# Optimization experiments

Measured on AMD Instinct MI355X. Metric: run time of the kernel, lower is better.

## Reference

```python
import jax, jax.numpy as jnp
import numpy as np

DIM_Q, DIM_K, HEADS = 256, 32, 4
SCALE = (DIM_Q // HEADS) ** (-0.5)


def setup_inputs() -> dict:
    key = jax.random.key(0)
    ks = jax.random.split(key, 12)
    B, C, H, W, D = 2, DIM_Q, 16, 16, 16
    inp = {
        'F_VNet': jax.random.normal(ks[0], (B, C, H, W, D), dtype=jnp.float32),
        'F_Knowledge': jax.random.normal(ks[1], (B, DIM_K, H, W, D), dtype=jnp.float32),
        # torch nn.Linear: y = x @ W.T + b, W: [out, in]
        'Wq': jax.random.normal(ks[2], (DIM_Q, DIM_Q), dtype=jnp.float32) * (DIM_Q ** -0.5),
        'bq': jnp.zeros((DIM_Q,), dtype=jnp.float32),
        'Wk': jax.random.normal(ks[3], (DIM_Q, DIM_K), dtype=jnp.float32) * (DIM_K ** -0.5),
        'bk': jnp.zeros((DIM_Q,), dtype=jnp.float32),
        'Wv': jax.random.normal(ks[4], (DIM_Q, DIM_K), dtype=jnp.float32) * (DIM_K ** -0.5),
        'bv': jnp.zeros((DIM_Q,), dtype=jnp.float32),
        'Wo': jax.random.normal(ks[5], (DIM_Q, DIM_Q), dtype=jnp.float32) * (DIM_Q ** -0.5),
        'bo': jnp.zeros((DIM_Q,), dtype=jnp.float32),
    }
    return inp


def reference(F_VNet, F_Knowledge, Wq, bq, Wk, bk, Wv, bv, Wo, bo):
    B, C, H, W, D = F_VNet.shape
    Ck = F_Knowledge.shape[1]
    # flatten spatial dims to tokens: [B, N, C]
    xq = F_VNet.reshape(B, C, -1).transpose(0, 2, 1)          # [B, Nq, dim_q]
    xk = F_Knowledge.reshape(B, Ck, -1).transpose(0, 2, 1)    # [B, Nk, dim_k]
    Q = xq @ Wq.T + bq                                        # [B, Nq, dim_q]
    K = xk @ Wk.T + bk                                        # [B, Nk, dim_q]
    V = xk @ Wv.T + bv                                        # [B, Nk, dim_q]
    attn = jax.nn.softmax(jnp.einsum('bqc,bkc->bqk', Q, K) * SCALE, axis=-1)
    out = jnp.einsum('bqk,bkc->bqc', attn, V)                 # [B, Nq, dim_q]
    out = out @ Wo.T + bo
    out = out.transpose(0, 2, 1).reshape(B, C, H, W, D)
    return F_VNet + out
```

## Files before the change

kernel.cpp:

```cpp
#include <hip/hip_runtime.h>
#include <hip/hip_bf16.h>
#include <cstdint>
#include <cstddef>

#define N_TOK 4096
#define CQ    256
#define CK    32
#define QK_SCALE 0.18033688011112042f

typedef __attribute__((ext_vector_type(4))) float  f32x4;
typedef __attribute__((ext_vector_type(8))) __bf16 bf16x8;
typedef __attribute__((ext_vector_type(4))) short  s16x4;

__device__ __forceinline__ unsigned short f2bf(float f) {
  union { float f; unsigned u; } x; x.f = f;
  unsigned r = x.u + 0x7FFFu + ((x.u >> 16) & 1u);
  return (unsigned short)(r >> 16);
}

__device__ __forceinline__ f32x4 mfma16(bf16x8 a, bf16x8 b, f32x4 c) {
  return __builtin_amdgcn_mfma_f32_16x16x32_bf16(a, b, c, 0, 0, 0);
}

__device__ __forceinline__ float exp2fast(float x) {
#if __has_builtin(__builtin_amdgcn_exp2f)
  return __builtin_amdgcn_exp2f(x);
#else
  float r; asm("v_exp_f32 %0, %1" : "=v"(r) : "v"(x)); return r;
#endif
}

__device__ __forceinline__ void bar_lds() {
  asm volatile("s_waitcnt lgkmcnt(0)" ::: "memory");
  __builtin_amdgcn_s_barrier();
}

__device__ __forceinline__ int pos2key(int pos) {
  return ((pos >> 3) << 2) + (pos & 3) + (((pos >> 2) & 1) << 4);
}

__global__ __launch_bounds__(256) void prep_kernel(
    const float* __restrict__ Wq, const float* __restrict__ bq,
    const float* __restrict__ Wk, const float* __restrict__ Wv,
    const float* __restrict__ bv, const float* __restrict__ Wo,
    const float* __restrict__ bo, const float* __restrict__ Fk,
    unsigned short* __restrict__ Aqkt, float* __restrict__ bqk,
    unsigned short* __restrict__ W2bf, float* __restrict__ c2,
    unsigned short* __restrict__ Vpv, unsigned short* __restrict__ XkT)
{
  __shared__ float red[256];
  __shared__ unsigned short trs[128][33];
  const int blk = blockIdx.x, t = threadIdx.x;
  if (blk < 32) {
    const int j = blk;
    float acc = 0.f;
    #pragma unroll 16
    for (int i = 0; i < CQ; i++)
      acc = fmaf(Wq[(size_t)i * CQ + t], Wk[(size_t)i * CK + j], acc);
    Aqkt[(size_t)j * CQ + t] = f2bf(QK_SCALE * acc);
    red[t] = bq[t] * Wk[(size_t)t * CK + j];
    __syncthreads();
    for (int s = 128; s > 0; s >>= 1) {
      if (t < s) red[t] += red[t + s];
      __syncthreads();
    }
    if (t == 0) bqk[j] = QK_SCALE * red[0];
  } else if (blk < 64) {
    const int j = blk - 32;
    float acc = 0.f, acc2 = 0.f;
    #pragma unroll 16
    for (int i = 0; i < CQ; i++) {
      float wo = Wo[(size_t)t * CQ + i];
      acc  = fmaf(wo, Wv[(size_t)i * CK + j], acc);
      acc2 = fmaf(wo, bv[i], acc2);
    }
    W2bf[(size_t)t * CK + j] = f2bf(acc);
    if (j == 0) c2[t] = bo[t] + acc2;
  } else {
    const int blk2 = blk - 64;
    const int b = blk2 >> 5;
    const int t0 = (blk2 & 31) << 7;
    #pragma unroll
    for (int i = 0; i < 4; i++) {
      int flat = (i * 256 + t) << 2;
      int r = flat >> 7, c4 = flat & 127;
      float4 v = *(const float4*)(Fk + ((size_t)(b * CK + r)) * N_TOK + t0 + c4);
      ushort4 u = { f2bf(v.x), f2bf(v.y), f2bf(v.z), f2bf(v.w) };
      trs[c4][r] = u.x; trs[c4+1][r] = u.y; trs[c4+2][r] = u.z; trs[c4+3][r] = u.w;
    }
    __syncthreads();
    {
      const int token = t >> 1, half = t & 1;
      unsigned short tmp[16] __attribute__((aligned(16)));
      #pragma unroll
      for (int k = 0; k < 16; k++) tmp[k] = trs[token][half * 16 + k];
      unsigned short* dst = XkT + ((size_t)(b * N_TOK + t0 + token)) * CK + half * 16;
      ((uint4*)dst)[0] = ((const uint4*)tmp)[0];
      ((uint4*)dst)[1] = ((const uint4*)tmp)[1];
    }
    {
      const int ch32l = t >> 6, d = (t & 63) >> 1, ph = t & 1;
      unsigned short tmp[16] __attribute__((aligned(16)));
      #pragma unroll
      for (int i = 0; i < 16; i++) {
        int pos = ph * 16 + i;
        tmp[i] = trs[ch32l * 32 + pos2key(pos)][d];
      }
      unsigned short* dst = Vpv +
          (((size_t)(b * 128 + (t0 >> 5) + ch32l)) * 32 + d) * 32 + ph * 16;
      ((uint4*)dst)[0] = ((const uint4*)tmp)[0];
      ((uint4*)dst)[1] = ((const uint4*)tmp)[1];
    }
  }
}

__global__ __launch_bounds__(256, 1) void fused_kernel(
    const float* __restrict__ X, const unsigned short* __restrict__ Aqkt,
    const float* __restrict__ bqk, const unsigned short* __restrict__ XkT,
    const unsigned short* __restrict__ Vpv,
    const unsigned short* __restrict__ W2bf, const float* __restrict__ c2,
    float* __restrict__ Y)
{
  __shared__ union {
    unsigned short ks[512 * 40];
    unsigned short bs8[8][32][40];
  } u __attribute__((aligned(16)));
  __shared__ unsigned short qn[32][40] __attribute__((aligned(16)));
  __shared__ float mlx[2][2][16];
  __shared__ float ofx[2][16][32];

  const int b  = blockIdx.x >> 7;
  const int t0 = (blockIdx.x & 127) << 5;
  const int t = threadIdx.x, w = t >> 6;
  const int lane = t & 63, c = lane & 15, g = lane >> 4;
  const int tw = w & 1, kh = w >> 1;
  const int pk = kh << 8;

  #pragma unroll
  for (int i = 0; i < 8; i++) {
    int flat = i * 256 + t;
    int cc = flat >> 3, tk = (flat & 7) << 2;
    float4 v = *(const float4*)(X + ((size_t)(b * CQ + cc)) * N_TOK + t0 + tk);
    int kk = cc >> 5, chl = cc & 31;
    u.bs8[kk][tk    ][chl] = f2bf(v.x);
    u.bs8[kk][tk + 1][chl] = f2bf(v.y);
    u.bs8[kk][tk + 2][chl] = f2bf(v.z);
    u.bs8[kk][tk + 3][chl] = f2bf(v.w);
  }
  const unsigned short* xksrc = XkT + ((size_t)b * N_TOK) * CK;
  uint4 R[8];
  #pragma unroll
  for (int r = 0; r < 8; r++)
    R[r] = *(const uint4*)(xksrc + (size_t)(r * 256 + t) * 8);
  bar_lds();

  if (w < 2) {
    f32x4 qacc[2] = {};
    #pragma unroll
    for (int kk = 0; kk < 8; kk++) {
      bf16x8 a = *(const bf16x8*)&u.bs8[kk][w * 16 + c][g * 8];
      #pragma unroll
      for (int nt = 0; nt < 2; nt++) {
        bf16x8 bB = *(const bf16x8*)(Aqkt + (size_t)(nt * 16 + c) * CQ + kk * 32 + g * 8);
        qacc[nt] = mfma16(a, bB, qacc[nt]);
      }
    }
    #pragma unroll
    for (int nt = 0; nt < 2; nt++) {
      float bj = bqk[nt * 16 + c];
      #pragma unroll
      for (int r = 0; r < 4; r++)
        qn[w * 16 + g * 4 + r][nt * 16 + c] = f2bf(qacc[nt][r] + bj);
    }
  }
  bar_lds();

  const bf16x8 qf = *(const bf16x8*)&qn[tw * 16 + c][g * 8];
  const unsigned short* vp = Vpv + (size_t)b * 128 * 1024;

  float mO = -1e30f, lO = 0.f;
  f32x4 O0 = {}, O1 = {};

  for (int s = 0; s < 8; s++) {
    #pragma unroll
    for (int r = 0; r < 8; r++) {
      int flat = r * 256 + t;
      *(uint4*)(u.ks + (flat >> 2) * 40 + (flat & 3) * 8) = R[r];
    }
    if (s < 7) {
      const unsigned short* nsrc = xksrc + (size_t)(s + 1) * (512 * CK);
      #pragma unroll
      for (int r = 0; r < 8; r++)
        R[r] = *(const uint4*)(nsrc + (size_t)(r * 256 + t) * 8);
    }
    bar_lds();

    f32x4 sc[4][4];
    #pragma unroll
    for (int it = 0; it < 4; it++)
      #pragma unroll
      for (int nt = 0; nt < 4; nt++) {
        bf16x8 ak = *(const bf16x8*)&u.ks[(pk + it * 64 + nt * 16 + c) * 40 + g * 8];
        f32x4 z = {};
        sc[it][nt] = mfma16(ak, qf, z);
      }

    float mx = -1e30f;
    #pragma unroll
    for (int it = 0; it < 4; it++)
      #pragma unroll
      for (int nt = 0; nt < 4; nt++)
        mx = fmaxf(mx, fmaxf(fmaxf(sc[it][nt][0], sc[it][nt][1]),
                             fmaxf(sc[it][nt][2], sc[it][nt][3])));
    mx = fmaxf(mx, __shfl_xor(mx, 16));
    mx = fmaxf(mx, __shfl_xor(mx, 32));

    float l = 0.f;
    s16x4 pf[4][4];
    #pragma unroll
    for (int it = 0; it < 4; it++)
      #pragma unroll
      for (int nt = 0; nt < 4; nt++) {
        float p0 = exp2fast(sc[it][nt][0] - mx);
        float p1 = exp2fast(sc[it][nt][1] - mx);
        float p2 = exp2fast(sc[it][nt][2] - mx);
        float p3 = exp2fast(sc[it][nt][3] - mx);
        l += (p0 + p1) + (p2 + p3);
        union { __hip_bfloat162 h2[2]; s16x4 v; } pu;
        pu.h2[0] = __float22bfloat162_rn(make_float2(p0, p1));
        pu.h2[1] = __float22bfloat162_rn(make_float2(p2, p3));
        pf[it][nt] = pu.v;
      }
    l += __shfl_xor(l, 16);
    l += __shfl_xor(l, 32);

    f32x4 o0 = {}, o1 = {};
    #pragma unroll
    for (int it = 0; it < 4; it++)
      #pragma unroll
      for (int ntp = 0; ntp < 2; ntp++) {
        const int ch32 = (s << 4) + (kh << 3) + it * 2 + ntp;
        const unsigned short* base = vp + (size_t)ch32 * 1024;
        union { s16x4 h[2]; bf16x8 v; } bu;
        bu.h[0] = pf[it][ntp * 2];
        bu.h[1] = pf[it][ntp * 2 + 1];
        bf16x8 a0 = *(const bf16x8*)(base + c * 32 + g * 8);
        bf16x8 a1 = *(const bf16x8*)(base + (16 + c) * 32 + g * 8);
        o0 = mfma16(a0, bu.v, o0);
        o1 = mfma16(a1, bu.v, o1);
      }

    float mN = fmaxf(mO, mx);
    float fO = exp2fast(mO - mN), fP = exp2fast(mx - mN);
    lO = lO * fO + l * fP;
    #pragma unroll
    for (int r = 0; r < 4; r++) {
      O0[r] = O0[r] * fO + o0[r] * fP;
      O1[r] = O1[r] * fO + o1[r] * fP;
    }
    mO = mN;
    bar_lds();
  }

  if (kh == 1) {
    if (lane < 16) { mlx[tw][0][c] = mO; mlx[tw][1][c] = lO; }
    #pragma unroll
    for (int r = 0; r < 4; r++) {
      ofx[tw][c][g * 4 + r]      = O0[r];
      ofx[tw][c][16 + g * 4 + r] = O1[r];
    }
  }
  __syncthreads();
  if (kh == 0) {
    float m1 = mlx[tw][0][c], l1 = mlx[tw][1][c];
    float mN = fmaxf(mO, m1);
    float f0 = exp2fast(mO - mN), f1 = exp2fast(m1 - mN);
    float inv = 1.0f / (lO * f0 + l1 * f1);
    f0 *= inv; f1 *= inv;
    #pragma unroll
    for (int r = 0; r < 4; r++) {
      qn[tw * 16 + c][g * 4 + r]      = f2bf(O0[r] * f0 + ofx[tw][c][g * 4 + r] * f1);
      qn[tw * 16 + c][16 + g * 4 + r] = f2bf(O1[r] * f0 + ofx[tw][c][16 + g * 4 + r] * f1);
    }
  }
  __syncthreads();

  const int m0 = w * 64;
  bf16x8 wb[2];
  #pragma unroll
  for (int nt = 0; nt < 2; nt++)
    wb[nt] = *(const bf16x8*)&qn[nt * 16 + c][g * 8];
  f32x4 acc2[4][2] = {};
  #pragma unroll
  for (int mt = 0; mt < 4; mt++) {
    bf16x8 aW = *(const bf16x8*)(W2bf + (size_t)(m0 + mt * 16 + c) * CK + g * 8);
    acc2[mt][0] = mfma16(aW, wb[0], acc2[mt][0]);
    acc2[mt][1] = mfma16(aW, wb[1], acc2[mt][1]);
  }
  #pragma unroll
  for (int mt = 0; mt < 4; mt++)
    #pragma unroll
    for (int r = 0; r < 4; r++) {
      const int row = m0 + mt * 16 + g * 4 + r;
      const float cc2 = c2[row];
      #pragma unroll
      for (int nt = 0; nt < 2; nt++) {
        size_t idx = ((size_t)(b * CQ + row)) * N_TOK + t0 + nt * 16 + c;
        Y[idx] = acc2[mt][nt][r] + cc2 + X[idx];
      }
    }
}

extern "C" void kernel_launch(void* const* d_in, const int* in_sizes, int n_in,
                              void* d_out, int out_size, void* d_ws, size_t ws_size,
                              hipStream_t stream) {
  const float* F  = (const float*)d_in[0];
  const float* Fk = (const float*)d_in[1];
  const float* Wq = (const float*)d_in[2];
  const float* bq = (const float*)d_in[3];
  const float* Wk = (const float*)d_in[4];
  const float* Wv = (const float*)d_in[6];
  const float* bv = (const float*)d_in[7];
  const float* Wo = (const float*)d_in[8];
  const float* bo = (const float*)d_in[9];
  float* Y = (float*)d_out;
  char* ws = (char*)d_ws;
  unsigned short* XkT   = (unsigned short*)(ws);
  unsigned short* Vpv   = (unsigned short*)(ws + (512u << 10));
  unsigned short* Aqkt  = (unsigned short*)(ws + (2048u << 10));
  unsigned short* W2bf  = (unsigned short*)(ws + (2080u << 10));
  float*          bqk   = (float*)(ws + (2112u << 10));
  float*          c2    = (float*)(ws + (2116u << 10));

  prep_kernel <<<128, 256, 0, stream>>>(Wq, bq, Wk, Wv, bv, Wo, bo, Fk,
                                        Aqkt, bqk, W2bf, c2, Vpv, XkT);
  fused_kernel<<<256, 256, 0, stream>>>(F, Aqkt, bqk, XkT, Vpv, W2bf, c2, Y);
}
```

Baseline: 120.6 us.

## Split keys across four waves with 16-query blocks and drop LDS K staging

Each block now handles 16 query tokens instead of 32, doubling the grid to 512 blocks. The four waves each take a quarter of the keys and read K fragments straight from global memory instead of staging them in LDS with barriers. The four partial softmax states are merged through LDS at the end. This cuts LDS use and per-iteration synchronisation to raise occupancy and parallelism, at the cost of redundant Q projection in every wave and uncoalesced global loads of X and K.

```diff
diff --git a/kernel.cpp b/kernel.cpp
--- a/kernel.cpp
+++ b/kernel.cpp
@@ -28,11 +28,6 @@
 #else
   float r; asm("v_exp_f32 %0, %1" : "=v"(r) : "v"(x)); return r;
 #endif
-}
-
-__device__ __forceinline__ void bar_lds() {
-  asm volatile("s_waitcnt lgkmcnt(0)" ::: "memory");
-  __builtin_amdgcn_s_barrier();
 }
 
 __device__ __forceinline__ int pos2key(int pos) {
@@ -114,93 +109,60 @@
   }
 }
 
-__global__ __launch_bounds__(256, 1) void fused_kernel(
+__global__ __launch_bounds__(256, 2) void fused_kernel(
     const float* __restrict__ X, const unsigned short* __restrict__ Aqkt,
     const float* __restrict__ bqk, const unsigned short* __restrict__ XkT,
     const unsigned short* __restrict__ Vpv,
     const unsigned short* __restrict__ W2bf, const float* __restrict__ c2,
     float* __restrict__ Y)
 {
-  __shared__ union {
-    unsigned short ks[512 * 40];
-    unsigned short bs8[8][32][40];
-  } u __attribute__((aligned(16)));
-  __shared__ unsigned short qn[32][40] __attribute__((aligned(16)));
-  __shared__ float mlx[2][2][16];
-  __shared__ float ofx[2][16][32];
-
-  const int b  = blockIdx.x >> 7;
-  const int t0 = (blockIdx.x & 127) << 5;
+  __shared__ unsigned short qn[16][40] __attribute__((aligned(16)));
+  __shared__ float ml[4][2][16];
+  __shared__ float ow[4][16][34];
+
+  const int b  = blockIdx.x >> 8;
+  const int t0 = (blockIdx.x & 255) << 4;
   const int t = threadIdx.x, w = t >> 6;
   const int lane = t & 63, c = lane & 15, g = lane >> 4;
-  const int tw = w & 1, kh = w >> 1;
-  const int pk = kh << 8;
-
-  #pragma unroll
-  for (int i = 0; i < 8; i++) {
-    int flat = i * 256 + t;
-    int cc = flat >> 3, tk = (flat & 7) << 2;
-    float4 v = *(const float4*)(X + ((size_t)(b * CQ + cc)) * N_TOK + t0 + tk);
-    int kk = cc >> 5, chl = cc & 31;
-    u.bs8[kk][tk    ][chl] = f2bf(v.x);
-    u.bs8[kk][tk + 1][chl] = f2bf(v.y);
-    u.bs8[kk][tk + 2][chl] = f2bf(v.z);
-    u.bs8[kk][tk + 3][chl] = f2bf(v.w);
-  }
-  const unsigned short* xksrc = XkT + ((size_t)b * N_TOK) * CK;
-  uint4 R[8];
-  #pragma unroll
-  for (int r = 0; r < 8; r++)
-    R[r] = *(const uint4*)(xksrc + (size_t)(r * 256 + t) * 8);
-  bar_lds();
-
-  if (w < 2) {
-    f32x4 qacc[2] = {};
-    #pragma unroll
-    for (int kk = 0; kk < 8; kk++) {
-      bf16x8 a = *(const bf16x8*)&u.bs8[kk][w * 16 + c][g * 8];
-      #pragma unroll
-      for (int nt = 0; nt < 2; nt++) {
-        bf16x8 bB = *(const bf16x8*)(Aqkt + (size_t)(nt * 16 + c) * CQ + kk * 32 + g * 8);
-        qacc[nt] = mfma16(a, bB, qacc[nt]);
-      }
-    }
+
+  f32x4 qacc[2] = {};
+  #pragma unroll
+  for (int kk = 0; kk < 8; kk++) {
+    const float* xb = X + ((size_t)(b * CQ + kk * 32 + g * 8)) * N_TOK + t0 + c;
+    union { unsigned short u[8]; bf16x8 v; } a;
+    #pragma unroll
+    for (int j = 0; j < 8; j++) a.u[j] = f2bf(xb[(size_t)j * N_TOK]);
+    #pragma unroll
+    for (int nt = 0; nt < 2; nt++) {
+      bf16x8 bB = *(const bf16x8*)(Aqkt + (size_t)(nt * 16 + c) * CQ + kk * 32 + g * 8);
+      qacc[nt] = mfma16(a.v, bB, qacc[nt]);
+    }
+  }
+  if (w == 0) {
     #pragma unroll
     for (int nt = 0; nt < 2; nt++) {
       float bj = bqk[nt * 16 + c];
       #pragma unroll
       for (int r = 0; r < 4; r++)
-        qn[w * 16 + g * 4 + r][nt * 16 + c] = f2bf(qacc[nt][r] + bj);
-    }
-  }
-  bar_lds();
-
-  const bf16x8 qf = *(const bf16x8*)&qn[tw * 16 + c][g * 8];
+        qn[g * 4 + r][nt * 16 + c] = f2bf(qacc[nt][r] + bj);
+    }
+  }
+  __syncthreads();
+  const bf16x8 qf = *(const bf16x8*)&qn[c][g * 8];
+
+  const unsigned short* kb = XkT + ((size_t)(b * N_TOK + w * 1024)) * CK;
   const unsigned short* vp = Vpv + (size_t)b * 128 * 1024;
-
   float mO = -1e30f, lO = 0.f;
   f32x4 O0 = {}, O1 = {};
 
-  for (int s = 0; s < 8; s++) {
-    #pragma unroll
-    for (int r = 0; r < 8; r++) {
-      int flat = r * 256 + t;
-      *(uint4*)(u.ks + (flat >> 2) * 40 + (flat & 3) * 8) = R[r];
-    }
-    if (s < 7) {
-      const unsigned short* nsrc = xksrc + (size_t)(s + 1) * (512 * CK);
-      #pragma unroll
-      for (int r = 0; r < 8; r++)
-        R[r] = *(const uint4*)(nsrc + (size_t)(r * 256 + t) * 8);
-    }
-    bar_lds();
-
+  for (int chb = 0; chb < 4; chb++) {
     f32x4 sc[4][4];
     #pragma unroll
     for (int it = 0; it < 4; it++)
       #pragma unroll
       for (int nt = 0; nt < 4; nt++) {
-        bf16x8 ak = *(const bf16x8*)&u.ks[(pk + it * 64 + nt * 16 + c) * 40 + g * 8];
+        bf16x8 ak = *(const bf16x8*)(kb +
+            (size_t)(chb * 256 + it * 64 + nt * 16 + c) * CK + g * 8);
         f32x4 z = {};
         sc[it][nt] = mfma16(ak, qf, z);
       }
@@ -239,7 +201,7 @@
     for (int it = 0; it < 4; it++)
       #pragma unroll
       for (int ntp = 0; ntp < 2; ntp++) {
-        const int ch32 = (s << 4) + (kh << 3) + it * 2 + ntp;
+        const int ch32 = w * 32 + chb * 8 + it * 2 + ntp;
         const unsigned short* base = vp + (size_t)ch32 * 1024;
         union { s16x4 h[2]; bf16x8 v; } bu;
         bu.h[0] = pf[it][ntp * 2];
@@ -259,55 +221,53 @@
       O1[r] = O1[r] * fO + o1[r] * fP;
     }
     mO = mN;
-    bar_lds();
-  }
-
-  if (kh == 1) {
-    if (lane < 16) { mlx[tw][0][c] = mO; mlx[tw][1][c] = lO; }
-    #pragma unroll
-    for (int r = 0; r < 4; r++) {
-      ofx[tw][c][g * 4 + r]      = O0[r];
-      ofx[tw][c][16 + g * 4 + r] = O1[r];
-    }
+  }
+
+  if (lane < 16) { ml[w][0][c] = mO; ml[w][1][c] = lO; }
+  #pragma unroll
+  for (int r = 0; r < 4; r++) {
+    ow[w][c][g * 4 + r]      = O0[r];
+    ow[w][c][16 + g * 4 + r] = O1[r];
   }
   __syncthreads();
-  if (kh == 0) {
-    float m1 = mlx[tw][0][c], l1 = mlx[tw][1][c];
-    float mN = fmaxf(mO, m1);
-    float f0 = exp2fast(mO - mN), f1 = exp2fast(m1 - mN);
-    float inv = 1.0f / (lO * f0 + l1 * f1);
-    f0 *= inv; f1 *= inv;
-    #pragma unroll
-    for (int r = 0; r < 4; r++) {
-      qn[tw * 16 + c][g * 4 + r]      = f2bf(O0[r] * f0 + ofx[tw][c][g * 4 + r] * f1);
-      qn[tw * 16 + c][16 + g * 4 + r] = f2bf(O1[r] * f0 + ofx[tw][c][16 + g * 4 + r] * f1);
-    }
-  }
-  __syncthreads();
+
+  float m4[4], l4[4], mM = -1e30f;
+  #pragma unroll
+  for (int k = 0; k < 4; k++) {
+    m4[k] = ml[k][0][c]; l4[k] = ml[k][1][c];
+    mM = fmaxf(mM, m4[k]);
+  }
+  float f4[4], ls = 0.f;
+  #pragma unroll
+  for (int k = 0; k < 4; k++) {
+    f4[k] = exp2fast(m4[k] - mM);
+    ls = fmaf(f4[k], l4[k], ls);
+  }
+  const float inv = 1.0f / ls;
+  union { unsigned short u[8]; bf16x8 v; } wb;
+  #pragma unroll
+  for (int j = 0; j < 8; j++) {
+    float acc = 0.f;
+    #pragma unroll
+    for (int k = 0; k < 4; k++)
+      acc = fmaf(f4[k], ow[k][c][g * 8 + j], acc);
+    wb.u[j] = f2bf(acc * inv);
+  }
 
   const int m0 = w * 64;
-  bf16x8 wb[2];
-  #pragma unroll
-  for (int nt = 0; nt < 2; nt++)
-    wb[nt] = *(const bf16x8*)&qn[nt * 16 + c][g * 8];
-  f32x4 acc2[4][2] = {};
+  f32x4 acc2[4] = {};
   #pragma unroll
   for (int mt = 0; mt < 4; mt++) {
     bf16x8 aW = *(const bf16x8*)(W2bf + (size_t)(m0 + mt * 16 + c) * CK + g * 8);
-    acc2[mt][0] = mfma16(aW, wb[0], acc2[mt][0]);
-    acc2[mt][1] = mfma16(aW, wb[1], acc2[mt][1]);
+    acc2[mt] = mfma16(aW, wb.v, acc2[mt]);
   }
   #pragma unroll
   for (int mt = 0; mt < 4; mt++)
     #pragma unroll
     for (int r = 0; r < 4; r++) {
       const int row = m0 + mt * 16 + g * 4 + r;
-      const float cc2 = c2[row];
-      #pragma unroll
-      for (int nt = 0; nt < 2; nt++) {
-        size_t idx = ((size_t)(b * CQ + row)) * N_TOK + t0 + nt * 16 + c;
-        Y[idx] = acc2[mt][nt][r] + cc2 + X[idx];
-      }
+      size_t idx = ((size_t)(b * CQ + row)) * N_TOK + t0 + c;
+      Y[idx] = acc2[mt][r] + c2[row] + X[idx];
     }
 }
 
@@ -334,5 +294,5 @@
 
   prep_kernel <<<128, 256, 0, stream>>>(Wq, bq, Wk, Wv, bv, Wo, bo, Fk,
                                         Aqkt, bqk, W2bf, c2, Vpv, XkT);
-  fused_kernel<<<256, 256, 0, stream>>>(F, Aqkt, bqk, XkT, Vpv, W2bf, c2, Y);
-}
+  fused_kernel<<<512, 256, 0, stream>>>(F, Aqkt, bqk, XkT, Vpv, W2bf, c2, Y);
+}
```

New measurement: 118.0 us. 1.02x faster.
